# Performance work log

Hardware: AMD Instinct MI355X
Metric: run time of the kernel (lower is better)

The kernel has to match this reference:

```python
import jax, jax.numpy as jnp
import numpy as np
from jax import lax

B, L, C = 8, 2048, 512
CR = C // 4      # SE reduction hidden
DH = C // 2      # fusion d_hidden
KS = [3, 7, 15, 20]
EPS = 1e-5


def _ln(x, g, b):
    m = jnp.mean(x, -1, keepdims=True)
    v = jnp.mean((x - m) ** 2, -1, keepdims=True)
    return (x - m) / jnp.sqrt(v + EPS) * g + b


def _bn(x, g, b, m, v):  # x: [B,C,L], eval-mode BatchNorm1d
    return (x - m[:, None]) / jnp.sqrt(v[:, None] + EPS) * g[:, None] + b[:, None]


def _forward(x, pw_w, pw_b, pw_bn_g, pw_bn_b, pw_bn_m, pw_bn_v,
             dw_w0, dw_w1, dw_w2, dw_w3, dw_b, dw_bn_g, dw_bn_b, dw_bn_m, dw_bn_v,
             se_w1, se_b1, se_w2, se_b2, se_ln_g, se_ln_b,
             df_ln_g, df_ln_b, wq, bq, wv, bv, wg, bg,
             op_w, op_b, op_ln_g, op_ln_b, fn_g, fn_b):
    Bs, Ls, Cs = x.shape
    x_in = jnp.transpose(x, (0, 2, 1))                      # [B,C,L]
    # pointwise conv (1x1) + BN + ReLU
    x_pw = jnp.einsum('oc,bcl->bol', pw_w, x_in) + pw_b[:, None]
    x_pw = jax.nn.relu(_bn(x_pw, pw_bn_g, pw_bn_b, pw_bn_m, pw_bn_v))

    enhanced = []
    for i, (w, k) in enumerate(zip([dw_w0, dw_w1, dw_w2, dw_w3], KS)):
        p = (k - 1) // 2
        y = lax.conv_general_dilated(
            x_pw, w[:, None, :], window_strides=(1,), padding=[(p, p)],
            feature_group_count=Cs, dimension_numbers=('NCH', 'OIH', 'NCH'))
        y = y + dw_b[i][:, None]
        y = jax.nn.relu(_bn(y, dw_bn_g[i], dw_bn_b[i], dw_bn_m[i], dw_bn_v[i]))
        if y.shape[2] > Ls:
            y = y[:, :, :Ls]
        elif y.shape[2] < Ls:
            y = jnp.pad(y, ((0, 0), (0, 0), (0, Ls - y.shape[2])))
        feat = jnp.transpose(y, (0, 2, 1))                  # [B,L,C]
        # ChannelAttentionBlock (SE): pool over L -> MLP -> sigmoid gate -> residual LN
        ym = jnp.mean(feat, axis=1)                          # [B,C]
        h = jax.nn.relu(ym @ se_w1[i].T + se_b1[i])          # [B,CR]
        wt = jax.nn.sigmoid(h @ se_w2[i].T + se_b2[i])       # [B,C]
        enhanced.append(_ln(feat + feat * wt[:, None, :], se_ln_g[i], se_ln_b[i]))

    # diff_conv: fixed weight w[:,:,0]=-1, w[:,:,1]=1 => every out channel is
    # sum_c(x[l+1,c]-x[l,c]); pad one zero step at the end
    s = jnp.sum(x[:, 1:] - x[:, :-1], axis=-1, keepdims=True)    # [B,L-1,1]
    diff_feat = jnp.pad(jnp.broadcast_to(s, (Bs, Ls - 1, Cs)), ((0, 0), (0, 1), (0, 0)))

    # DiffGuidedInteractiveFusion
    D = _ln(diff_feat, df_ln_g, df_ln_b)
    Q = D @ wq.T + bq                                       # [B,L,DH]
    scores = []
    for f in enhanced:
        Vi = f @ wv.T + bv                                  # [B,L,DH]
        scores.append(jnp.tanh(Q * Vi) @ wg + bg)           # [B,L]
    scores = jnp.stack(scores, axis=-1)                     # [B,L,S]
    sw = jax.nn.softmax(scores, axis=-1)
    fused = sum(sw[..., i:i + 1] * enhanced[i] for i in range(len(enhanced)))
    out = _ln(fused @ op_w.T + op_b, op_ln_g, op_ln_b)
    return _ln(out + x, fn_g, fn_b)


def setup_inputs() -> dict:
    key = jax.random.key(0)
    ks = jax.random.split(key, 12)
    r = lambda k, s: jax.random.normal(k, s, jnp.float32) * 0.02
    return {
        'x': jax.random.normal(ks[0], (B, L, C), jnp.float32),
        'pw_w': r(ks[1], (C, C)), 'pw_b': jnp.zeros(C),
        'pw_bn_g': jnp.ones(C), 'pw_bn_b': jnp.zeros(C), 'pw_bn_m': jnp.zeros(C), 'pw_bn_v': jnp.ones(C),
        'dw_w0': r(ks[2], (C, 3)), 'dw_w1': r(ks[3], (C, 7)), 'dw_w2': r(ks[4], (C, 15)), 'dw_w3': r(ks[5], (C, 20)),
        'dw_b': jnp.zeros((4, C)),
        'dw_bn_g': jnp.ones((4, C)), 'dw_bn_b': jnp.zeros((4, C)), 'dw_bn_m': jnp.zeros((4, C)), 'dw_bn_v': jnp.ones((4, C)),
        'se_w1': r(ks[6], (4, CR, C)), 'se_b1': jnp.zeros((4, CR)),
        'se_w2': r(ks[7], (4, C, CR)), 'se_b2': jnp.zeros((4, C)),
        'se_ln_g': jnp.ones((4, C)), 'se_ln_b': jnp.zeros((4, C)),
        'df_ln_g': jnp.ones(C), 'df_ln_b': jnp.zeros(C),
        'wq': r(ks[8], (DH, C)), 'bq': jnp.zeros(DH),
        'wv': r(ks[9], (DH, C)), 'bv': jnp.zeros(DH),
        'wg': r(ks[10], (DH,)), 'bg': jnp.zeros(()),
        'op_w': r(ks[11], (C, C)), 'op_b': jnp.zeros(C),
        'op_ln_g': jnp.ones(C), 'op_ln_b': jnp.zeros(C),
        'fn_g': jnp.ones(C), 'fn_b': jnp.zeros(C),
    }


def reference(x, pw_w, pw_b, pw_bn_g, pw_bn_b, pw_bn_m, pw_bn_v,
              dw_w0, dw_w1, dw_w2, dw_w3, dw_b, dw_bn_g, dw_bn_b, dw_bn_m, dw_bn_v,
              se_w1, se_b1, se_w2, se_b2, se_ln_g, se_ln_b,
              df_ln_g, df_ln_b, wq, bq, wv, bv, wg, bg,
              op_w, op_b, op_ln_g, op_ln_b, fn_g, fn_b):
    return _forward(x, pw_w, pw_b, pw_bn_g, pw_bn_b, pw_bn_m, pw_bn_v,
                    dw_w0, dw_w1, dw_w2, dw_w3, dw_b, dw_bn_g, dw_bn_b, dw_bn_m, dw_bn_v,
                    se_w1, se_b1, se_w2, se_b2, se_ln_g, se_ln_b,
                    df_ln_g, df_ln_b, wq, bq, wv, bv, wg, bg,
                    op_w, op_b, op_ln_g, op_ln_b, fn_g, fn_b)
```

## Files before the change

kernel.cpp:

```cpp
#include <hip/hip_runtime.h>
#include <math.h>

static constexpr int Bz = 8;
static constexpr int Lz = 2048;
static constexpr int Cz = 512;
static constexpr int CRz = 128;
static constexpr int DHz = 256;
static constexpr int MT = Bz * Lz;
static constexpr float EPSz = 1e-5f;

typedef unsigned short u16;
typedef __bf16 bf16x8 __attribute__((ext_vector_type(8)));
typedef float f32x4 __attribute__((ext_vector_type(4)));
typedef unsigned short u16x8 __attribute__((ext_vector_type(8)));

__device__ __forceinline__ float bf2f(u16 u) {
  unsigned int v = ((unsigned int)u) << 16;
  return __builtin_bit_cast(float, v);
}
__device__ __forceinline__ u16 f2bf(float f) {
  unsigned int b = __builtin_bit_cast(unsigned int, f);
  b += 0x7FFFu + ((b >> 16) & 1u);
  return (u16)(b >> 16);
}
__device__ __forceinline__ f32x4 mfma16(bf16x8 a, bf16x8 b, f32x4 c) {
  return __builtin_amdgcn_mfma_f32_16x16x32_bf16(a, b, c, 0, 0, 0);
}

__global__ __launch_bounds__(256) void cvt_bf16_kernel(
    const float* __restrict__ src, u16* __restrict__ dst, int n8) {
  int i = blockIdx.x * 256 + threadIdx.x;
  if (i >= n8) return;
  const float4* s = (const float4*)src;
  float4 a = s[i * 2], b = s[i * 2 + 1];
  u16x8 o;
  o[0] = f2bf(a.x); o[1] = f2bf(a.y); o[2] = f2bf(a.z); o[3] = f2bf(a.w);
  o[4] = f2bf(b.x); o[5] = f2bf(b.y); o[6] = f2bf(b.z); o[7] = f2bf(b.w);
  ((u16x8*)dst)[i] = o;
}

__global__ __launch_bounds__(256) void prep_kernel(
    const float* __restrict__ pw_b, const float* __restrict__ pw_g,
    const float* __restrict__ pw_bb, const float* __restrict__ pw_m,
    const float* __restrict__ pw_v,
    const float* __restrict__ dw_b, const float* __restrict__ dw_g,
    const float* __restrict__ dw_bb, const float* __restrict__ dw_m,
    const float* __restrict__ dw_v,
    const float* __restrict__ df_ln_b, const float* __restrict__ wq,
    const float* __restrict__ bq,
    float* __restrict__ pwA, float* __restrict__ pwB,
    float* __restrict__ dwA, float* __restrict__ dwB,
    float* __restrict__ qc) {
  const int blk = blockIdx.x;
  const int t = threadIdx.x;
  if (blk == 0) {
    for (int c = t; c < Cz; c += 256) {
      float inv = rsqrtf(pw_v[c] + EPSz);
      float a = pw_g[c] * inv;
      float bb = pw_bb[c] - pw_m[c] * a;
      pwA[c] = a;
      pwB[c] = pw_b[c] * a + bb;
    }
  } else if (blk <= 4) {
    const int i = blk - 1;
    for (int c = t; c < Cz; c += 256) {
      int idx = i * Cz + c;
      float inv = rsqrtf(dw_v[idx] + EPSz);
      float a = dw_g[idx] * inv;
      float bb = dw_bb[idx] - dw_m[idx] * a;
      dwA[idx] = a;
      dwB[idx] = dw_b[idx] * a + bb;
    }
  } else {
    if (t < DHz) {
      float s = bq[t];
      const float* w = wq + (size_t)t * Cz;
      for (int c = 0; c < Cz; c++) s += df_ln_b[c] * w[c];
      qc[t] = s;
    }
  }
}

__global__ __launch_bounds__(256, 2) void pw_mfma_kernel(
    const u16* __restrict__ Wbf, const float* __restrict__ x,
    const float* __restrict__ alpha, const float* __restrict__ beta,
    u16* __restrict__ xpw) {
  __shared__ __align__(16) char lds[74240];
  u16(*sX)[520] = (u16(*)[520])lds;
  u16(*sW)[40] = (u16(*)[40])(lds + 33280);
  u16* sC = (u16*)(lds + 33280);
  __shared__ float sAl[Cz];
  __shared__ float sBe[Cz];
  const int bat = blockIdx.x >> 6;
  const int l0 = (blockIdx.x & 63) * 32;
  const int t = threadIdx.x;
  const int lane = t & 63, w = t >> 6;
  const int fr = lane & 15, fk = (lane >> 4) * 8;
  const int mh = (w >> 1) * 16;
  const int nh = (w & 1) * 16;
#pragma unroll
  for (int rep = 0; rep < 8; rep++) {
    const int idx = rep * 256 + t;
    const int row = idx >> 6;
    const int col = (idx & 63) * 8;
    const float* src = x + ((size_t)bat * Lz + l0 + row) * Cz + col;
    float4 f0 = *(const float4*)src;
    float4 f1 = *(const float4*)(src + 4);
    u16x8 o;
    o[0] = f2bf(f0.x); o[1] = f2bf(f0.y); o[2] = f2bf(f0.z); o[3] = f2bf(f0.w);
    o[4] = f2bf(f1.x); o[5] = f2bf(f1.y); o[6] = f2bf(f1.z); o[7] = f2bf(f1.w);
    *(u16x8*)&sX[row][col] = o;
  }
  for (int c = t; c < Cz; c += 256) { sAl[c] = alpha[c]; sBe[c] = beta[c]; }
  f32x4 acc[16];
#pragma unroll
  for (int mf = 0; mf < 16; mf++)
#pragma unroll
    for (int r = 0; r < 4; r++) acc[mf][r] = 0.f;
  const int wrow = t >> 2, wch = (t & 3) * 8;
  const u16* wbase = Wbf + (size_t)wrow * Cz + wch;
  u16x8 breg[8];
#pragma unroll
  for (int rep = 0; rep < 8; rep++)
    breg[rep] = *(const u16x8*)(wbase + (size_t)rep * 64 * Cz);
  for (int k0 = 0; k0 < Cz; k0 += 32) {
    __syncthreads();
#pragma unroll
    for (int rep = 0; rep < 8; rep++)
      *(u16x8*)&sW[rep * 64 + wrow][wch] = breg[rep];
    __syncthreads();
    if (k0 + 32 < Cz) {
#pragma unroll
      for (int rep = 0; rep < 8; rep++)
        breg[rep] = *(const u16x8*)(wbase + (size_t)rep * 64 * Cz + k0 + 32);
    }
    bf16x8 bfrag = *(const bf16x8*)&sX[nh + fr][k0 + fk];
#pragma unroll
    for (int mf = 0; mf < 16; mf++) {
      bf16x8 a = *(const bf16x8*)&sW[(mh + mf) * 16 + fr][fk];
      acc[mf] = mfma16(a, bfrag, acc[mf]);
    }
  }
  __syncthreads();
#pragma unroll
  for (int mf = 0; mf < 16; mf++) {
#pragma unroll
    for (int r = 0; r < 4; r++) {
      const int o = (mh + mf) * 16 + ((lane >> 4) << 2) + r;
      const int l = nh + fr;
      float v = fmaxf(acc[mf][r] * sAl[o] + sBe[o], 0.f);
      sC[o * 40 + l] = f2bf(v);
    }
  }
  __syncthreads();
#pragma unroll
  for (int rep = 0; rep < 8; rep++) {
    const int o = rep * 64 + (t >> 2);
    const int l8 = (t & 3) * 8;
    u16x8 v = *(const u16x8*)&sC[o * 40 + l8];
    *(u16x8*)(xpw + ((size_t)(bat * Cz + o)) * Lz + l0 + l8) = v;
  }
}

template <int K>
__device__ __forceinline__ float dw_branch(const float* __restrict__ row,
                                           const float* __restrict__ wts,
                                           float a, float bb, int valid, int t,
                                           u16* __restrict__ dst) {
  constexpr int P = (K - 1) / 2;
  constexpr int W = 8 + K - 1;
  float wreg[K];
#pragma unroll
  for (int j = 0; j < K; j++) wreg[j] = wts[j];
  const int base = t * 8 - P;
  float win[W];
  if (base >= 0 && base + W <= Lz) {
#pragma unroll
    for (int j = 0; j < W; j++) {
      const int idx = base + j;
      win[j] = row[idx + (idx >> 5)];
    }
  } else {
#pragma unroll
    for (int j = 0; j < W; j++) {
      const int idx = base + j;
      win[j] = (idx >= 0 && idx < Lz) ? row[idx + (idx >> 5)] : 0.f;
    }
  }
  float acc[8] = {};
#pragma unroll
  for (int jj = 0; jj < K; jj++)
#pragma unroll
    for (int o = 0; o < 8; o++) acc[o] = fmaf(wreg[jj], win[jj + o], acc[o]);
  u16x8 ov;
  float psum = 0.f;
#pragma unroll
  for (int o = 0; o < 8; o++) {
    float v = fmaxf(acc[o] * a + bb, 0.f);
    if (t * 8 + o >= valid) v = 0.f;
    ov[o] = f2bf(v);
    psum += v;
  }
  *(u16x8*)(dst + t * 8) = ov;
  return psum;
}

__global__ __launch_bounds__(256) void dw_conv_kernel(
    const u16* __restrict__ xpw,
    const float* __restrict__ w0, const float* __restrict__ w1,
    const float* __restrict__ w2, const float* __restrict__ w3,
    const float* __restrict__ dwA, const float* __restrict__ dwB,
    u16* __restrict__ y, float* __restrict__ ysum) {
  __shared__ float row[Lz + Lz / 32];
  __shared__ float wts[48];
  __shared__ float wsum[4][4];
  const int b = blockIdx.x >> 9;
  const int c = blockIdx.x & 511;
  const int t = threadIdx.x;
  const size_t NBL = (size_t)Bz * Cz * Lz;
  {
    u16x8 v = ((const u16x8*)(xpw + ((size_t)(b * Cz + c)) * Lz))[t];
#pragma unroll
    for (int j = 0; j < 8; j++) {
      const int idx = t * 8 + j;
      row[idx + (idx >> 5)] = bf2f(v[j]);
    }
  }
  if (t < 45) {
    float wv;
    if (t < 3) wv = w0[c * 3 + t];
    else if (t < 10) wv = w1[c * 7 + (t - 3)];
    else if (t < 25) wv = w2[c * 15 + (t - 10)];
    else wv = w3[c * 20 + (t - 25)];
    wts[t] = wv;
  }
  __syncthreads();
  u16* dstb = y + ((size_t)b * Cz + c) * Lz;
  float ps[4];
  ps[0] = dw_branch<3>(row, wts + 0, dwA[c], dwB[c], Lz, t, dstb);
  ps[1] = dw_branch<7>(row, wts + 3, dwA[Cz + c], dwB[Cz + c], Lz, t,
                       dstb + NBL);
  ps[2] = dw_branch<15>(row, wts + 10, dwA[2 * Cz + c], dwB[2 * Cz + c], Lz, t,
                        dstb + 2 * NBL);
  ps[3] = dw_branch<20>(row, wts + 25, dwA[3 * Cz + c], dwB[3 * Cz + c],
                        Lz - 1, t, dstb + 3 * NBL);
#pragma unroll
  for (int off = 32; off > 0; off >>= 1) {
#pragma unroll
    for (int i = 0; i < 4; i++) ps[i] += __shfl_down(ps[i], off, 64);
  }
  if ((t & 63) == 0) {
#pragma unroll
    for (int i = 0; i < 4; i++) wsum[t >> 6][i] = ps[i];
  }
  __syncthreads();
  if (t < 4)
    ysum[(t * Bz + b) * Cz + c] =
        wsum[0][t] + wsum[1][t] + wsum[2][t] + wsum[3][t];
}

__global__ __launch_bounds__(128) void se_kernel(
    const float* __restrict__ ysum,
    const float* __restrict__ se_w1, const float* __restrict__ se_b1,
    const float* __restrict__ se_w2, const float* __restrict__ se_b2,
    float* __restrict__ sc) {
  const int i = blockIdx.x >> 3;
  const int b = blockIdx.x & 7;
  __shared__ float ym[Cz];
  __shared__ float h[CRz];
  const int t = threadIdx.x;
  const float* ys = ysum + (i * Bz + b) * Cz;
  for (int cc = t; cc < Cz; cc += 128) ym[cc] = ys[cc] * (1.f / Lz);
  __syncthreads();
  {
    const float* w1 = se_w1 + (size_t)i * CRz * Cz + (size_t)t * Cz;
    float s = se_b1[i * CRz + t];
    for (int cc = 0; cc < Cz; cc++) s += ym[cc] * w1[cc];
    h[t] = fmaxf(s, 0.f);
  }
  __syncthreads();
  for (int cc = t; cc < Cz; cc += 128) {
    const float* w2 = se_w2 + ((size_t)i * Cz + cc) * CRz;
    float s = se_b2[i * Cz + cc];
    for (int r = 0; r < CRz; r++) s += h[r] * w2[r];
    float wt = 1.f / (1.f + expf(-s));
    sc[(i * Bz + b) * Cz + cc] = 1.f + wt;
  }
}

__global__ __launch_bounds__(256) void ln_transpose_kernel(
    const u16* __restrict__ ybuf, const float* __restrict__ scv,
    const float* __restrict__ se_ln_g, const float* __restrict__ se_ln_b,
    u16* __restrict__ ebuf) {
  __shared__ float tile[32][Cz + 1];
  const size_t NBL = (size_t)Bz * Cz * Lz;
  const int i = blockIdx.y >> 3;
  const int b = blockIdx.y & 7;
  const int l0 = blockIdx.x * 32;
  const int t = threadIdx.x;
  const u16* yb = ybuf + (size_t)i * NBL + (size_t)b * Cz * Lz;
  const float* scb = scv + (i * Bz + b) * Cz;
  const float* g = se_ln_g + i * Cz;
  const float* bb = se_ln_b + i * Cz;
#pragma unroll
  for (int rep = 0; rep < 8; rep++) {
    const int idx = rep * 256 + t;
    const int c = idx >> 2;
    const int l8 = (idx & 3) * 8;
    u16x8 v = *(const u16x8*)(yb + (size_t)c * Lz + l0 + l8);
    const float scale = scb[c];
#pragma unroll
    for (int j = 0; j < 8; j++) tile[l8 + j][c] = bf2f(v[j]) * scale;
  }
  __syncthreads();
  const int wave = t >> 6, lane = t & 63;
  u16* eb = ebuf + (size_t)i * NBL + ((size_t)b * Lz + l0) * Cz;
  for (int r = wave; r < 32; r += 4) {
    float vals[8];
    float s1 = 0.f, s2 = 0.f;
#pragma unroll
    for (int j = 0; j < 8; j++) {
      float v = tile[r][lane + j * 64];
      vals[j] = v; s1 += v; s2 += v * v;
    }
    for (int off = 32; off > 0; off >>= 1) {
      s1 += __shfl_xor(s1, off, 64);
      s2 += __shfl_xor(s2, off, 64);
    }
    const float m = s1 * (1.f / Cz);
    const float var = s2 * (1.f / Cz) - m * m;
    const float inv = rsqrtf(var + EPSz);
#pragma unroll
    for (int j = 0; j < 8; j++) {
      const int cc = lane + j * 64;
      eb[(size_t)r * Cz + cc] = f2bf((vals[j] - m) * inv * g[cc] + bb[cc]);
    }
  }
}

__global__ __launch_bounds__(256) void score_mfma_kernel(
    const u16* __restrict__ e0, const u16* __restrict__ e1,
    const u16* __restrict__ e2, const u16* __restrict__ e3,
    const u16* __restrict__ wvbf, const float* __restrict__ bv,
    const float* __restrict__ qc, const float* __restrict__ wg,
    const float* __restrict__ bg, float* __restrict__ scores) {
  __shared__ u16 sA[64][40];
  __shared__ u16 sB[256][40];
  __shared__ float sP[4][64];
  const int i = blockIdx.y;
  const u16* E = (i == 0) ? e0 : (i == 1) ? e1 : (i == 2) ? e2 : e3;
  const int r0 = blockIdx.x * 64;
  const int t = threadIdx.x;
  const int lane = t & 63, w = t >> 6;
  const int srow = t >> 2, skoff = (t & 3) * 8;
  const int fr = lane & 15, fk = (lane >> 4) * 8;
  const u16* ap = E + (size_t)(r0 + srow) * Cz + skoff;
  const u16* bp = wvbf + (size_t)srow * Cz + skoff;
  f32x4 acc[4][4];
#pragma unroll
  for (int m = 0; m < 4; m++)
#pragma unroll
    for (int j = 0; j < 4; j++)
#pragma unroll
      for (int r = 0; r < 4; r++) acc[m][j][r] = 0.f;
  for (int k0 = 0; k0 < Cz; k0 += 32) {
    u16x8 av = *(const u16x8*)(ap + k0);
    u16x8 bq0 = *(const u16x8*)(bp + k0);
    u16x8 bq1 = *(const u16x8*)(bp + (size_t)64 * Cz + k0);
    u16x8 bq2 = *(const u16x8*)(bp + (size_t)128 * Cz + k0);
    u16x8 bq3 = *(const u16x8*)(bp + (size_t)192 * Cz + k0);
    __syncthreads();
    *(u16x8*)&sA[srow][skoff] = av;
    *(u16x8*)&sB[srow][skoff] = bq0;
    *(u16x8*)&sB[srow + 64][skoff] = bq1;
    *(u16x8*)&sB[srow + 128][skoff] = bq2;
    *(u16x8*)&sB[srow + 192][skoff] = bq3;
    __syncthreads();
    bf16x8 am[4], bj[4];
#pragma unroll
    for (int m = 0; m < 4; m++) am[m] = *(const bf16x8*)&sA[m * 16 + fr][fk];
#pragma unroll
    for (int j = 0; j < 4; j++)
      bj[j] = *(const bf16x8*)&sB[(w * 4 + j) * 16 + fr][fk];
#pragma unroll
    for (int m = 0; m < 4; m++)
#pragma unroll
      for (int j = 0; j < 4; j++)
        acc[m][j] = mfma16(am[m], bj[j], acc[m][j]);
  }
  float part[4][4];
#pragma unroll
  for (int m = 0; m < 4; m++)
#pragma unroll
    for (int r = 0; r < 4; r++) part[m][r] = 0.f;
#pragma unroll
  for (int j = 0; j < 4; j++) {
    const int dh = (w * 4 + j) * 16 + fr;
    const float bvn = bv[dh], qcn = qc[dh], wgn = wg[dh];
#pragma unroll
    for (int m = 0; m < 4; m++)
#pragma unroll
      for (int r = 0; r < 4; r++)
        part[m][r] += tanhf(qcn * (acc[m][j][r] + bvn)) * wgn;
  }
#pragma unroll
  for (int off = 1; off < 16; off <<= 1) {
#pragma unroll
    for (int m = 0; m < 4; m++)
#pragma unroll
      for (int r = 0; r < 4; r++)
        part[m][r] += __shfl_xor(part[m][r], off, 64);
  }
  if (fr == 0) {
#pragma unroll
    for (int m = 0; m < 4; m++)
#pragma unroll
      for (int r = 0; r < 4; r++)
        sP[w][m * 16 + ((lane >> 4) << 2) + r] = part[m][r];
  }
  __syncthreads();
  if (t < 64) {
    float s = sP[0][t] + sP[1][t] + sP[2][t] + sP[3][t] + bg[0];
    scores[(size_t)i * MT + r0 + t] = s;
  }
}

__global__ __launch_bounds__(256, 2) void op_mfma_kernel(
    const u16* __restrict__ e0, const u16* __restrict__ e1,
    const u16* __restrict__ e2, const u16* __restrict__ e3,
    const float* __restrict__ scores, const u16* __restrict__ opwbf,
    const float* __restrict__ opb, u16* __restrict__ oproj) {
  __shared__ u16 sA[32][520];
  __shared__ u16 sB[512][40];
  __shared__ float sw4[4][32];
  const int m0 = blockIdx.x * 32;
  const int t = threadIdx.x;
  const int lane = t & 63, w = t >> 6;
  const int fr = lane & 15, fk = (lane >> 4) * 8;
  const int mh = (w >> 1) * 16;
  const int nh = (w & 1) * 16;
  if (t < 32) {
    const int r = m0 + t;
    float s0 = scores[r], s1 = scores[MT + r], s2 = scores[2 * MT + r],
          s3 = scores[3 * MT + r];
    float mx = fmaxf(fmaxf(s0, s1), fmaxf(s2, s3));
    float x0 = expf(s0 - mx), x1 = expf(s1 - mx), x2 = expf(s2 - mx),
          x3 = expf(s3 - mx);
    float inv = 1.f / (x0 + x1 + x2 + x3);
    sw4[0][t] = x0 * inv; sw4[1][t] = x1 * inv;
    sw4[2][t] = x2 * inv; sw4[3][t] = x3 * inv;
  }
  __syncthreads();
#pragma unroll
  for (int rep = 0; rep < 8; rep++) {
    const int idx = rep * 256 + t;
    const int row = idx >> 6;
    const int col = (idx & 63) * 8;
    const size_t off = (size_t)(m0 + row) * Cz + col;
    u16x8 v0 = *(const u16x8*)(e0 + off);
    u16x8 v1 = *(const u16x8*)(e1 + off);
    u16x8 v2 = *(const u16x8*)(e2 + off);
    u16x8 v3 = *(const u16x8*)(e3 + off);
    const float x0 = sw4[0][row], x1 = sw4[1][row], x2 = sw4[2][row],
                x3 = sw4[3][row];
    u16x8 o;
#pragma unroll
    for (int j = 0; j < 8; j++)
      o[j] = f2bf(x0 * bf2f(v0[j]) + x1 * bf2f(v1[j]) + x2 * bf2f(v2[j]) +
                  x3 * bf2f(v3[j]));
    *(u16x8*)&sA[row][col] = o;
  }
  f32x4 acc[16];
#pragma unroll
  for (int nf = 0; nf < 16; nf++)
#pragma unroll
    for (int r = 0; r < 4; r++) acc[nf][r] = 0.f;
  const int wrow = t >> 2, wch = (t & 3) * 8;
  const u16* wbase = opwbf + (size_t)wrow * Cz + wch;
  u16x8 breg[8];
#pragma unroll
  for (int rep = 0; rep < 8; rep++)
    breg[rep] = *(const u16x8*)(wbase + (size_t)rep * 64 * Cz);
  for (int k0 = 0; k0 < Cz; k0 += 32) {
    __syncthreads();
#pragma unroll
    for (int rep = 0; rep < 8; rep++)
      *(u16x8*)&sB[rep * 64 + wrow][wch] = breg[rep];
    __syncthreads();
    if (k0 + 32 < Cz) {
#pragma unroll
      for (int rep = 0; rep < 8; rep++)
        breg[rep] = *(const u16x8*)(wbase + (size_t)rep * 64 * Cz + k0 + 32);
    }
    bf16x8 a = *(const bf16x8*)&sA[mh + fr][k0 + fk];
#pragma unroll
    for (int nf = 0; nf < 16; nf++) {
      bf16x8 b = *(const bf16x8*)&sB[(nh + nf) * 16 + fr][fk];
      acc[nf] = mfma16(a, b, acc[nf]);
    }
  }
  __syncthreads();
  u16* sC = (u16*)&sA[0][0];
#pragma unroll
  for (int nf = 0; nf < 16; nf++) {
    const int n = (nh + nf) * 16 + fr;
    const float ob = opb[n];
#pragma unroll
    for (int r = 0; r < 4; r++) {
      const int row = mh + ((lane >> 4) << 2) + r;
      sC[row * 520 + n] = f2bf(acc[nf][r] + ob);
    }
  }
  __syncthreads();
#pragma unroll
  for (int rep = 0; rep < 8; rep++) {
    const int idx = rep * 256 + t;
    const int row = idx >> 6;
    const int col = (idx & 63) * 8;
    u16x8 v = *(const u16x8*)&sC[row * 520 + col];
    *(u16x8*)(oproj + (size_t)(m0 + row) * Cz + col) = v;
  }
}

__global__ __launch_bounds__(256) void final_ln_kernel(
    const u16* __restrict__ oproj, const float* __restrict__ g1,
    const float* __restrict__ b1, const float* __restrict__ x,
    const float* __restrict__ g2, const float* __restrict__ b2,
    float* __restrict__ out) {
  const int t = threadIdx.x;
  const int row = blockIdx.x * 4 + (t >> 6);
  const int lane = t & 63;
  u16x8 av = ((const u16x8*)(oproj + (size_t)row * Cz))[lane];
  float v[8];
  float s1 = 0.f, s2 = 0.f;
#pragma unroll
  for (int j = 0; j < 8; j++) {
    v[j] = bf2f(av[j]);
    s1 += v[j]; s2 += v[j] * v[j];
  }
  for (int off = 1; off < 64; off <<= 1) {
    s1 += __shfl_xor(s1, off, 64);
    s2 += __shfl_xor(s2, off, 64);
  }
  const float m1 = s1 * (1.f / Cz);
  const float iv1 = rsqrtf(s2 * (1.f / Cz) - m1 * m1 + EPSz);
  float4 g1a = ((const float4*)g1)[lane * 2], g1b = ((const float4*)g1)[lane * 2 + 1];
  float4 b1a = ((const float4*)b1)[lane * 2], b1b = ((const float4*)b1)[lane * 2 + 1];
  const float* xr = x + (size_t)row * Cz;
  float4 xa = ((const float4*)xr)[lane * 2], xb = ((const float4*)xr)[lane * 2 + 1];
  float gv[8] = {g1a.x, g1a.y, g1a.z, g1a.w, g1b.x, g1b.y, g1b.z, g1b.w};
  float bvv[8] = {b1a.x, b1a.y, b1a.z, b1a.w, b1b.x, b1b.y, b1b.z, b1b.w};
  float xv[8] = {xa.x, xa.y, xa.z, xa.w, xb.x, xb.y, xb.z, xb.w};
  float tv[8];
  s1 = 0.f; s2 = 0.f;
#pragma unroll
  for (int j = 0; j < 8; j++) {
    tv[j] = (v[j] - m1) * iv1 * gv[j] + bvv[j] + xv[j];
    s1 += tv[j]; s2 += tv[j] * tv[j];
  }
  for (int off = 1; off < 64; off <<= 1) {
    s1 += __shfl_xor(s1, off, 64);
    s2 += __shfl_xor(s2, off, 64);
  }
  const float m2 = s1 * (1.f / Cz);
  const float iv2 = rsqrtf(s2 * (1.f / Cz) - m2 * m2 + EPSz);
  float4 g2a = ((const float4*)g2)[lane * 2], g2b = ((const float4*)g2)[lane * 2 + 1];
  float4 b2a = ((const float4*)b2)[lane * 2], b2b = ((const float4*)b2)[lane * 2 + 1];
  float g2v[8] = {g2a.x, g2a.y, g2a.z, g2a.w, g2b.x, g2b.y, g2b.z, g2b.w};
  float b2v[8] = {b2a.x, b2a.y, b2a.z, b2a.w, b2b.x, b2b.y, b2b.z, b2b.w};
  float4 oa, ob;
  oa.x = (tv[0] - m2) * iv2 * g2v[0] + b2v[0];
  oa.y = (tv[1] - m2) * iv2 * g2v[1] + b2v[1];
  oa.z = (tv[2] - m2) * iv2 * g2v[2] + b2v[2];
  oa.w = (tv[3] - m2) * iv2 * g2v[3] + b2v[3];
  ob.x = (tv[4] - m2) * iv2 * g2v[4] + b2v[4];
  ob.y = (tv[5] - m2) * iv2 * g2v[5] + b2v[5];
  ob.z = (tv[6] - m2) * iv2 * g2v[6] + b2v[6];
  ob.w = (tv[7] - m2) * iv2 * g2v[7] + b2v[7];
  float* orow = out + (size_t)row * Cz;
  ((float4*)orow)[lane * 2] = oa;
  ((float4*)orow)[lane * 2 + 1] = ob;
}

extern "C" void kernel_launch(void* const* d_in, const int* in_sizes, int n_in,
                              void* d_out, int out_size, void* d_ws,
                              size_t ws_size, hipStream_t stream) {
  const float* x = (const float*)d_in[0];
  const float* pw_w = (const float*)d_in[1];
  const float* pw_b = (const float*)d_in[2];
  const float* pw_bn_g = (const float*)d_in[3];
  const float* pw_bn_b = (const float*)d_in[4];
  const float* pw_bn_m = (const float*)d_in[5];
  const float* pw_bn_v = (const float*)d_in[6];
  const float* dw_w0 = (const float*)d_in[7];
  const float* dw_w1 = (const float*)d_in[8];
  const float* dw_w2 = (const float*)d_in[9];
  const float* dw_w3 = (const float*)d_in[10];
  const float* dw_b = (const float*)d_in[11];
  const float* dw_bn_g = (const float*)d_in[12];
  const float* dw_bn_b = (const float*)d_in[13];
  const float* dw_bn_m = (const float*)d_in[14];
  const float* dw_bn_v = (const float*)d_in[15];
  const float* se_w1 = (const float*)d_in[16];
  const float* se_b1 = (const float*)d_in[17];
  const float* se_w2 = (const float*)d_in[18];
  const float* se_b2 = (const float*)d_in[19];
  const float* se_ln_g = (const float*)d_in[20];
  const float* se_ln_b = (const float*)d_in[21];
  const float* df_ln_b = (const float*)d_in[23];
  const float* wq = (const float*)d_in[24];
  const float* bq = (const float*)d_in[25];
  const float* wv = (const float*)d_in[26];
  const float* bv = (const float*)d_in[27];
  const float* wg = (const float*)d_in[28];
  const float* bg = (const float*)d_in[29];
  const float* op_w = (const float*)d_in[30];
  const float* op_b = (const float*)d_in[31];
  const float* op_ln_g = (const float*)d_in[32];
  const float* op_ln_b = (const float*)d_in[33];
  const float* fn_g = (const float*)d_in[34];
  const float* fn_b = (const float*)d_in[35];
  float* out = (float*)d_out;

  const size_t NBL = (size_t)Bz * Cz * Lz;
  char* p = (char*)d_ws;
  u16* oproj = (u16*)p; p += NBL * 2;
  u16* xpw = (u16*)p; p += NBL * 2;
  u16* ybuf = (u16*)p; p += 4 * NBL * 2;
  u16* ebuf = (u16*)p; p += 4 * NBL * 2;
  u16* pwwbf = (u16*)p; p += (size_t)Cz * Cz * 2;
  u16* wvbf = (u16*)p; p += (size_t)DHz * Cz * 2;
  u16* opwbf = (u16*)p; p += (size_t)Cz * Cz * 2;
  float* fbuf = (float*)p;
  float* ysum = fbuf;
  float* scv = fbuf + 16384;
  float* scores = fbuf + 32768;
  float* pwA = fbuf + 98304;
  float* pwB = pwA + 512;
  float* dwA = pwB + 512;
  float* dwB = dwA + 2048;
  float* qc = dwB + 2048;

  cvt_bf16_kernel<<<Cz * Cz / 8 / 256, 256, 0, stream>>>(pw_w, pwwbf,
                                                         Cz * Cz / 8);
  cvt_bf16_kernel<<<DHz * Cz / 8 / 256, 256, 0, stream>>>(wv, wvbf,
                                                          DHz * Cz / 8);
  cvt_bf16_kernel<<<Cz * Cz / 8 / 256, 256, 0, stream>>>(op_w, opwbf,
                                                         Cz * Cz / 8);

  prep_kernel<<<6, 256, 0, stream>>>(pw_b, pw_bn_g, pw_bn_b, pw_bn_m, pw_bn_v,
                                     dw_b, dw_bn_g, dw_bn_b, dw_bn_m, dw_bn_v,
                                     df_ln_b, wq, bq, pwA, pwB, dwA, dwB, qc);

  pw_mfma_kernel<<<Bz * (Lz / 32), 256, 0, stream>>>(pwwbf, x, pwA, pwB, xpw);

  dw_conv_kernel<<<Bz * Cz, 256, 0, stream>>>(xpw, dw_w0, dw_w1, dw_w2, dw_w3,
                                              dwA, dwB, ybuf, ysum);

  se_kernel<<<32, 128, 0, stream>>>(ysum, se_w1, se_b1, se_w2, se_b2, scv);

  ln_transpose_kernel<<<dim3(Lz / 32, 4 * Bz), 256, 0, stream>>>(
      ybuf, scv, se_ln_g, se_ln_b, ebuf);

  score_mfma_kernel<<<dim3(MT / 64, 4), 256, 0, stream>>>(
      ebuf, ebuf + NBL, ebuf + 2 * NBL, ebuf + 3 * NBL, wvbf, bv, qc, wg, bg,
      scores);

  op_mfma_kernel<<<MT / 32, 256, 0, stream>>>(
      ebuf, ebuf + NBL, ebuf + 2 * NBL, ebuf + 3 * NBL, scores, opwbf, op_b,
      oproj);

  final_ln_kernel<<<MT / 4, 256, 0, stream>>>(oproj, op_ln_g, op_ln_b, x, fn_g,
                                              fn_b, out);
}
```

Baseline: 236.4 us.

## Fuse final LayerNorms into op GEMM, prefetch score GEMM, bf16 LN tile

Three separate changes. First, the two final LayerNorms and the residual add move into the op projection kernel's epilogue, so the bf16 oproj intermediate is no longer written to and read back from global memory, and one launch is removed. Second, the score GEMM uses a K-step of 64 with register prefetch of the next tile, so global loads overlap the MFMA work and there are fewer barriers. Third, the LN-transpose kernel stages bf16 instead of fp32 in shared memory and keeps scale, gamma and beta in registers, which halves its LDS footprint. The trade-off is more register pressure and a longer serial epilogue in the op kernel.

```diff
diff --git a/kernel.cpp b/kernel.cpp
--- a/kernel.cpp
+++ b/kernel.cpp
@@ -292,7 +292,8 @@
     const u16* __restrict__ ybuf, const float* __restrict__ scv,
     const float* __restrict__ se_ln_g, const float* __restrict__ se_ln_b,
     u16* __restrict__ ebuf) {
-  __shared__ float tile[32][Cz + 1];
+  __shared__ u16 tile[32][522];
+  __shared__ float ssc[Cz];
   const size_t NBL = (size_t)Bz * Cz * Lz;
   const int i = blockIdx.y >> 3;
   const int b = blockIdx.y & 7;
@@ -300,27 +301,35 @@
   const int t = threadIdx.x;
   const u16* yb = ybuf + (size_t)i * NBL + (size_t)b * Cz * Lz;
   const float* scb = scv + (i * Bz + b) * Cz;
-  const float* g = se_ln_g + i * Cz;
-  const float* bb = se_ln_b + i * Cz;
+  for (int cc = t; cc < Cz; cc += 256) ssc[cc] = scb[cc];
 #pragma unroll
   for (int rep = 0; rep < 8; rep++) {
     const int idx = rep * 256 + t;
     const int c = idx >> 2;
     const int l8 = (idx & 3) * 8;
     u16x8 v = *(const u16x8*)(yb + (size_t)c * Lz + l0 + l8);
-    const float scale = scb[c];
-#pragma unroll
-    for (int j = 0; j < 8; j++) tile[l8 + j][c] = bf2f(v[j]) * scale;
+#pragma unroll
+    for (int j = 0; j < 8; j++) tile[l8 + j][c] = v[j];
   }
   __syncthreads();
   const int wave = t >> 6, lane = t & 63;
+  const float* g = se_ln_g + i * Cz;
+  const float* bb = se_ln_b + i * Cz;
+  float sc8[8], g8[8], b8[8];
+#pragma unroll
+  for (int j = 0; j < 8; j++) {
+    const int cc = lane + j * 64;
+    sc8[j] = ssc[cc];
+    g8[j] = g[cc];
+    b8[j] = bb[cc];
+  }
   u16* eb = ebuf + (size_t)i * NBL + ((size_t)b * Lz + l0) * Cz;
   for (int r = wave; r < 32; r += 4) {
     float vals[8];
     float s1 = 0.f, s2 = 0.f;
 #pragma unroll
     for (int j = 0; j < 8; j++) {
-      float v = tile[r][lane + j * 64];
+      float v = bf2f(tile[r][lane + j * 64]) * sc8[j];
       vals[j] = v; s1 += v; s2 += v * v;
     }
     for (int off = 32; off > 0; off >>= 1) {
@@ -333,7 +342,7 @@
 #pragma unroll
     for (int j = 0; j < 8; j++) {
       const int cc = lane + j * 64;
-      eb[(size_t)r * Cz + cc] = f2bf((vals[j] - m) * inv * g[cc] + bb[cc]);
+      eb[(size_t)r * Cz + cc] = f2bf((vals[j] - m) * inv * g8[j] + b8[j]);
     }
   }
 }
@@ -344,18 +353,24 @@
     const u16* __restrict__ wvbf, const float* __restrict__ bv,
     const float* __restrict__ qc, const float* __restrict__ wg,
     const float* __restrict__ bg, float* __restrict__ scores) {
-  __shared__ u16 sA[64][40];
-  __shared__ u16 sB[256][40];
+  __shared__ u16 sA[64][72];
+  __shared__ u16 sB[256][72];
   __shared__ float sP[4][64];
   const int i = blockIdx.y;
   const u16* E = (i == 0) ? e0 : (i == 1) ? e1 : (i == 2) ? e2 : e3;
   const int r0 = blockIdx.x * 64;
   const int t = threadIdx.x;
   const int lane = t & 63, w = t >> 6;
-  const int srow = t >> 2, skoff = (t & 3) * 8;
   const int fr = lane & 15, fk = (lane >> 4) * 8;
-  const u16* ap = E + (size_t)(r0 + srow) * Cz + skoff;
-  const u16* bp = wvbf + (size_t)srow * Cz + skoff;
+  const int srow = t >> 3;
+  const int kc = (t & 7) * 8;
+  u16x8 areg[2], breg[8];
+#pragma unroll
+  for (int rep = 0; rep < 2; rep++)
+    areg[rep] = *(const u16x8*)(E + (size_t)(r0 + rep * 32 + srow) * Cz + kc);
+#pragma unroll
+  for (int rep = 0; rep < 8; rep++)
+    breg[rep] = *(const u16x8*)(wvbf + (size_t)(rep * 32 + srow) * Cz + kc);
   f32x4 acc[4][4];
 #pragma unroll
   for (int m = 0; m < 4; m++)
@@ -363,30 +378,40 @@
     for (int j = 0; j < 4; j++)
 #pragma unroll
       for (int r = 0; r < 4; r++) acc[m][j][r] = 0.f;
-  for (int k0 = 0; k0 < Cz; k0 += 32) {
-    u16x8 av = *(const u16x8*)(ap + k0);
-    u16x8 bq0 = *(const u16x8*)(bp + k0);
-    u16x8 bq1 = *(const u16x8*)(bp + (size_t)64 * Cz + k0);
-    u16x8 bq2 = *(const u16x8*)(bp + (size_t)128 * Cz + k0);
-    u16x8 bq3 = *(const u16x8*)(bp + (size_t)192 * Cz + k0);
+  for (int k0 = 0; k0 < Cz; k0 += 64) {
     __syncthreads();
-    *(u16x8*)&sA[srow][skoff] = av;
-    *(u16x8*)&sB[srow][skoff] = bq0;
-    *(u16x8*)&sB[srow + 64][skoff] = bq1;
-    *(u16x8*)&sB[srow + 128][skoff] = bq2;
-    *(u16x8*)&sB[srow + 192][skoff] = bq3;
+#pragma unroll
+    for (int rep = 0; rep < 2; rep++)
+      *(u16x8*)&sA[rep * 32 + srow][kc] = areg[rep];
+#pragma unroll
+    for (int rep = 0; rep < 8; rep++)
+      *(u16x8*)&sB[rep * 32 + srow][kc] = breg[rep];
     __syncthreads();
-    bf16x8 am[4], bj[4];
-#pragma unroll
-    for (int m = 0; m < 4; m++) am[m] = *(const bf16x8*)&sA[m * 16 + fr][fk];
-#pragma unroll
-    for (int j = 0; j < 4; j++)
-      bj[j] = *(const bf16x8*)&sB[(w * 4 + j) * 16 + fr][fk];
-#pragma unroll
-    for (int m = 0; m < 4; m++)
+    if (k0 + 64 < Cz) {
+#pragma unroll
+      for (int rep = 0; rep < 2; rep++)
+        areg[rep] = *(const u16x8*)(E + (size_t)(r0 + rep * 32 + srow) * Cz +
+                                    k0 + 64 + kc);
+#pragma unroll
+      for (int rep = 0; rep < 8; rep++)
+        breg[rep] = *(const u16x8*)(wvbf + (size_t)(rep * 32 + srow) * Cz +
+                                    k0 + 64 + kc);
+    }
+#pragma unroll
+    for (int ks = 0; ks < 2; ks++) {
+      bf16x8 am[4], bj[4];
+#pragma unroll
+      for (int m = 0; m < 4; m++)
+        am[m] = *(const bf16x8*)&sA[m * 16 + fr][ks * 32 + fk];
 #pragma unroll
       for (int j = 0; j < 4; j++)
-        acc[m][j] = mfma16(am[m], bj[j], acc[m][j]);
+        bj[j] = *(const bf16x8*)&sB[(w * 4 + j) * 16 + fr][ks * 32 + fk];
+#pragma unroll
+      for (int m = 0; m < 4; m++)
+#pragma unroll
+        for (int j = 0; j < 4; j++)
+          acc[m][j] = mfma16(am[m], bj[j], acc[m][j]);
+    }
   }
   float part[4][4];
 #pragma unroll
@@ -429,7 +454,11 @@
     const u16* __restrict__ e0, const u16* __restrict__ e1,
     const u16* __restrict__ e2, const u16* __restrict__ e3,
     const float* __restrict__ scores, const u16* __restrict__ opwbf,
-    const float* __restrict__ opb, u16* __restrict__ oproj) {
+    const float* __restrict__ opb,
+    const float* __restrict__ g1, const float* __restrict__ b1,
+    const float* __restrict__ x,
+    const float* __restrict__ g2, const float* __restrict__ b2,
+    float* __restrict__ out) {
   __shared__ u16 sA[32][520];
   __shared__ u16 sB[512][40];
   __shared__ float sw4[4][32];
@@ -512,74 +541,66 @@
     }
   }
   __syncthreads();
-#pragma unroll
-  for (int rep = 0; rep < 8; rep++) {
-    const int idx = rep * 256 + t;
-    const int row = idx >> 6;
-    const int col = (idx & 63) * 8;
-    u16x8 v = *(const u16x8*)&sC[row * 520 + col];
-    *(u16x8*)(oproj + (size_t)(m0 + row) * Cz + col) = v;
-  }
-}
-
-__global__ __launch_bounds__(256) void final_ln_kernel(
-    const u16* __restrict__ oproj, const float* __restrict__ g1,
-    const float* __restrict__ b1, const float* __restrict__ x,
-    const float* __restrict__ g2, const float* __restrict__ b2,
-    float* __restrict__ out) {
-  const int t = threadIdx.x;
-  const int row = blockIdx.x * 4 + (t >> 6);
-  const int lane = t & 63;
-  u16x8 av = ((const u16x8*)(oproj + (size_t)row * Cz))[lane];
-  float v[8];
-  float s1 = 0.f, s2 = 0.f;
-#pragma unroll
-  for (int j = 0; j < 8; j++) {
-    v[j] = bf2f(av[j]);
-    s1 += v[j]; s2 += v[j] * v[j];
-  }
-  for (int off = 1; off < 64; off <<= 1) {
-    s1 += __shfl_xor(s1, off, 64);
-    s2 += __shfl_xor(s2, off, 64);
-  }
-  const float m1 = s1 * (1.f / Cz);
-  const float iv1 = rsqrtf(s2 * (1.f / Cz) - m1 * m1 + EPSz);
-  float4 g1a = ((const float4*)g1)[lane * 2], g1b = ((const float4*)g1)[lane * 2 + 1];
-  float4 b1a = ((const float4*)b1)[lane * 2], b1b = ((const float4*)b1)[lane * 2 + 1];
-  const float* xr = x + (size_t)row * Cz;
-  float4 xa = ((const float4*)xr)[lane * 2], xb = ((const float4*)xr)[lane * 2 + 1];
-  float gv[8] = {g1a.x, g1a.y, g1a.z, g1a.w, g1b.x, g1b.y, g1b.z, g1b.w};
-  float bvv[8] = {b1a.x, b1a.y, b1a.z, b1a.w, b1b.x, b1b.y, b1b.z, b1b.w};
-  float xv[8] = {xa.x, xa.y, xa.z, xa.w, xb.x, xb.y, xb.z, xb.w};
-  float tv[8];
-  s1 = 0.f; s2 = 0.f;
-#pragma unroll
-  for (int j = 0; j < 8; j++) {
-    tv[j] = (v[j] - m1) * iv1 * gv[j] + bvv[j] + xv[j];
-    s1 += tv[j]; s2 += tv[j] * tv[j];
-  }
-  for (int off = 1; off < 64; off <<= 1) {
-    s1 += __shfl_xor(s1, off, 64);
-    s2 += __shfl_xor(s2, off, 64);
-  }
-  const float m2 = s1 * (1.f / Cz);
-  const float iv2 = rsqrtf(s2 * (1.f / Cz) - m2 * m2 + EPSz);
-  float4 g2a = ((const float4*)g2)[lane * 2], g2b = ((const float4*)g2)[lane * 2 + 1];
-  float4 b2a = ((const float4*)b2)[lane * 2], b2b = ((const float4*)b2)[lane * 2 + 1];
-  float g2v[8] = {g2a.x, g2a.y, g2a.z, g2a.w, g2b.x, g2b.y, g2b.z, g2b.w};
-  float b2v[8] = {b2a.x, b2a.y, b2a.z, b2a.w, b2b.x, b2b.y, b2b.z, b2b.w};
-  float4 oa, ob;
-  oa.x = (tv[0] - m2) * iv2 * g2v[0] + b2v[0];
-  oa.y = (tv[1] - m2) * iv2 * g2v[1] + b2v[1];
-  oa.z = (tv[2] - m2) * iv2 * g2v[2] + b2v[2];
-  oa.w = (tv[3] - m2) * iv2 * g2v[3] + b2v[3];
-  ob.x = (tv[4] - m2) * iv2 * g2v[4] + b2v[4];
-  ob.y = (tv[5] - m2) * iv2 * g2v[5] + b2v[5];
-  ob.z = (tv[6] - m2) * iv2 * g2v[6] + b2v[6];
-  ob.w = (tv[7] - m2) * iv2 * g2v[7] + b2v[7];
-  float* orow = out + (size_t)row * Cz;
-  ((float4*)orow)[lane * 2] = oa;
-  ((float4*)orow)[lane * 2 + 1] = ob;
+  float g1v[8], b1v[8], g2v[8], b2v[8];
+  {
+    float4 a0 = ((const float4*)g1)[lane * 2], a1 = ((const float4*)g1)[lane * 2 + 1];
+    float4 c0 = ((const float4*)b1)[lane * 2], c1 = ((const float4*)b1)[lane * 2 + 1];
+    float4 d0 = ((const float4*)g2)[lane * 2], d1 = ((const float4*)g2)[lane * 2 + 1];
+    float4 e0v = ((const float4*)b2)[lane * 2], e1v = ((const float4*)b2)[lane * 2 + 1];
+    g1v[0]=a0.x; g1v[1]=a0.y; g1v[2]=a0.z; g1v[3]=a0.w;
+    g1v[4]=a1.x; g1v[5]=a1.y; g1v[6]=a1.z; g1v[7]=a1.w;
+    b1v[0]=c0.x; b1v[1]=c0.y; b1v[2]=c0.z; b1v[3]=c0.w;
+    b1v[4]=c1.x; b1v[5]=c1.y; b1v[6]=c1.z; b1v[7]=c1.w;
+    g2v[0]=d0.x; g2v[1]=d0.y; g2v[2]=d0.z; g2v[3]=d0.w;
+    g2v[4]=d1.x; g2v[5]=d1.y; g2v[6]=d1.z; g2v[7]=d1.w;
+    b2v[0]=e0v.x; b2v[1]=e0v.y; b2v[2]=e0v.z; b2v[3]=e0v.w;
+    b2v[4]=e1v.x; b2v[5]=e1v.y; b2v[6]=e1v.z; b2v[7]=e1v.w;
+  }
+  for (int rr = 0; rr < 8; rr++) {
+    const int row = w * 8 + rr;
+    u16x8 av = *(const u16x8*)&sC[row * 520 + lane * 8];
+    float v[8];
+    float s1 = 0.f, s2 = 0.f;
+#pragma unroll
+    for (int j = 0; j < 8; j++) {
+      v[j] = bf2f(av[j]);
+      s1 += v[j]; s2 += v[j] * v[j];
+    }
+    for (int off = 1; off < 64; off <<= 1) {
+      s1 += __shfl_xor(s1, off, 64);
+      s2 += __shfl_xor(s2, off, 64);
+    }
+    const float m1 = s1 * (1.f / Cz);
+    const float iv1 = rsqrtf(s2 * (1.f / Cz) - m1 * m1 + EPSz);
+    const float* xr = x + (size_t)(m0 + row) * Cz;
+    float4 xa = ((const float4*)xr)[lane * 2], xb = ((const float4*)xr)[lane * 2 + 1];
+    float xv[8] = {xa.x, xa.y, xa.z, xa.w, xb.x, xb.y, xb.z, xb.w};
+    float tv[8];
+    s1 = 0.f; s2 = 0.f;
+#pragma unroll
+    for (int j = 0; j < 8; j++) {
+      tv[j] = (v[j] - m1) * iv1 * g1v[j] + b1v[j] + xv[j];
+      s1 += tv[j]; s2 += tv[j] * tv[j];
+    }
+    for (int off = 1; off < 64; off <<= 1) {
+      s1 += __shfl_xor(s1, off, 64);
+      s2 += __shfl_xor(s2, off, 64);
+    }
+    const float m2 = s1 * (1.f / Cz);
+    const float iv2 = rsqrtf(s2 * (1.f / Cz) - m2 * m2 + EPSz);
+    float4 oa, ob;
+    oa.x = (tv[0] - m2) * iv2 * g2v[0] + b2v[0];
+    oa.y = (tv[1] - m2) * iv2 * g2v[1] + b2v[1];
+    oa.z = (tv[2] - m2) * iv2 * g2v[2] + b2v[2];
+    oa.w = (tv[3] - m2) * iv2 * g2v[3] + b2v[3];
+    ob.x = (tv[4] - m2) * iv2 * g2v[4] + b2v[4];
+    ob.y = (tv[5] - m2) * iv2 * g2v[5] + b2v[5];
+    ob.z = (tv[6] - m2) * iv2 * g2v[6] + b2v[6];
+    ob.w = (tv[7] - m2) * iv2 * g2v[7] + b2v[7];
+    float* orow = out + (size_t)(m0 + row) * Cz;
+    ((float4*)orow)[lane * 2] = oa;
+    ((float4*)orow)[lane * 2 + 1] = ob;
+  }
 }
 
 extern "C" void kernel_launch(void* const* d_in, const int* in_sizes, int n_in,
@@ -624,7 +645,7 @@
 
   const size_t NBL = (size_t)Bz * Cz * Lz;
   char* p = (char*)d_ws;
-  u16* oproj = (u16*)p; p += NBL * 2;
+  p += NBL * 2;
   u16* xpw = (u16*)p; p += NBL * 2;
   u16* ybuf = (u16*)p; p += 4 * NBL * 2;
   u16* ebuf = (u16*)p; p += 4 * NBL * 2;
@@ -668,8 +689,5 @@
 
   op_mfma_kernel<<<MT / 32, 256, 0, stream>>>(
       ebuf, ebuf + NBL, ebuf + 2 * NBL, ebuf + 3 * NBL, scores, opwbf, op_b,
-      oproj);
-
-  final_ln_kernel<<<MT / 4, 256, 0, stream>>>(oproj, op_ln_g, op_ln_b, x, fn_g,
-                                              fn_b, out);
-}
+      op_ln_g, op_ln_b, x, fn_g, fn_b, out);
+}
```

Result: faster. 211.7 us (median of 2 runs) (-10.4%).
